# Performance work log

Hardware: AMD Instinct MI355X
Metric: run time of the kernel (lower is better)

Reference implementation:

```python
import jax, jax.numpy as jnp
import numpy as np

B, N, C, H = 1, 4096, 512, 8
S = 64  # sqrt(N), static


def setup_inputs() -> dict:
    key = jax.random.key(0)
    ks = jax.random.split(key, 4)
    d = C // H
    return {
        "x": jax.random.normal(ks[0], (B, N, C), dtype=jnp.float32),
        "num_heads": H,
        "bias": jnp.zeros((1,), dtype=jnp.float32),  # unused in original forward
        "scale": jnp.asarray(d ** -0.5, dtype=jnp.float32),
        "Wqkv": jax.random.normal(ks[1], (3 * C, C), dtype=jnp.float32) * (C ** -0.5),
        "bqkv": jnp.zeros((3 * C,), dtype=jnp.float32),
        "Wproj": jax.random.normal(ks[2], (C, C), dtype=jnp.float32) * (C ** -0.5),
        "bproj": jnp.zeros((C,), dtype=jnp.float32),
    }


def reference(x, num_heads, bias, scale, Wqkv, bqkv, Wproj, bproj):
    b, n, c = x.shape
    d = c // num_heads
    # fused QKV projection: [b, n, 3c] -> [3, b, h, n, d]
    qkv = (x @ Wqkv.T + bqkv).reshape(b, n, 3, num_heads, d).transpose(2, 0, 3, 1, 4)
    q, k, v = qkv[0] * scale, qkv[1], qkv[2]
    attn = jax.nn.softmax(jnp.einsum("bhnd,bhmd->bhnm", q, k), axis=-1)
    out = jnp.einsum("bhnm,bhmd->bhnd", attn, v)
    out = out.transpose(0, 2, 1, 3).reshape(b, n, c)
    out = out @ Wproj.T + bproj
    return out.reshape(b, S, S, c)
```

## Files before the change

kernel.cpp:

```cpp
#include <hip/hip_runtime.h>
#include <stdint.h>

#define NTOK 4096
#define CDIM 512
#define HEADS 8
#define DHEAD 64
#define PHEAD (NTOK * DHEAD)

typedef __bf16 bf16x8 __attribute__((ext_vector_type(8)));
typedef float f32x4 __attribute__((ext_vector_type(4)));

__device__ __forceinline__ unsigned short bfbits(float f) {
    return __builtin_bit_cast(unsigned short, (__bf16)f);
}

__device__ __forceinline__ f32x4 mfma32(bf16x8 a, bf16x8 b, f32x4 c) {
    return __builtin_amdgcn_mfma_f32_16x16x32_bf16(a, b, c, 0, 0, 0);
}

__global__ void cast3_k(const float* __restrict__ x, const float* __restrict__ wq,
                        const float* __restrict__ wp,
                        unsigned short* __restrict__ xb, unsigned short* __restrict__ wqb,
                        unsigned short* __restrict__ wpb) {
    const int b = blockIdx.x;
    const float* src; unsigned short* dst; int base;
    if (b < 2048)      { src = x;  dst = xb;  base = b * 1024; }
    else if (b < 2816) { src = wq; dst = wqb; base = (b - 2048) * 1024; }
    else               { src = wp; dst = wpb; base = (b - 2816) * 1024; }
    const int i = base + threadIdx.x * 4;
    const float4 v = *(const float4*)(src + i);
    ushort4 o;
    o.x = bfbits(v.x); o.y = bfbits(v.y); o.z = bfbits(v.z); o.w = bfbits(v.w);
    *(ushort4*)(dst + i) = o;
}

template<int MODE>
__global__ __launch_bounds__(256) void gemm_bt(
    const unsigned short* __restrict__ A,
    const unsigned short* __restrict__ Bm,
    const float* __restrict__ bias,
    const float* __restrict__ scale_p,
    unsigned short* __restrict__ qkv_out,
    float* __restrict__ c_out,
    int M, int Nn, int K)
{
    __shared__ __align__(16) unsigned short smem[64 * 136];
    unsigned short* lA = smem;
    unsigned short* lB = smem + 64 * 32;

    const int tid = threadIdx.x;
    const int mBase = blockIdx.y * 64, nBase = blockIdx.x * 128;
    const int lane = tid & 63, w = tid >> 6;
    const int l16 = lane & 15, quad = lane >> 4;

    f32x4 acc[4][2] = {};

    for (int kt = 0; kt < K; kt += 32) {
        __syncthreads();
        {
            const int fe = tid * 8;
            const int row = fe >> 5, col = fe & 31;
            *(uint4*)&lA[fe] = *(const uint4*)&A[(size_t)(mBase + row) * K + kt + col];
        }
#pragma unroll
        for (int i = 0; i < 2; ++i) {
            const int fe = (i * 256 + tid) * 8;
            const int row = fe >> 5, col = fe & 31;
            *(uint4*)&lB[fe] = *(const uint4*)&Bm[(size_t)(nBase + row) * K + kt + col];
        }
        __syncthreads();

        bf16x8 af[4], bfr[2];
#pragma unroll
        for (int i = 0; i < 4; ++i)
            af[i] = *(const bf16x8*)&lA[(i * 16 + l16) * 32 + quad * 8];
#pragma unroll
        for (int j = 0; j < 2; ++j)
            bfr[j] = *(const bf16x8*)&lB[(w * 32 + j * 16 + l16) * 32 + quad * 8];
#pragma unroll
        for (int i = 0; i < 4; ++i)
#pragma unroll
            for (int j = 0; j < 2; ++j)
                acc[i][j] = mfma32(af[i], bfr[j], acc[i][j]);
    }

    if (MODE == 1) {
#pragma unroll
        for (int i = 0; i < 4; ++i)
#pragma unroll
            for (int j = 0; j < 2; ++j)
#pragma unroll
                for (int r = 0; r < 4; ++r) {
                    const int grow = mBase + i * 16 + quad * 4 + r;
                    const int gcol = nBase + w * 32 + j * 16 + l16;
                    c_out[(size_t)grow * Nn + gcol] = acc[i][j][r] + bias[gcol];
                }
    } else {
        const int three = nBase >> 9;
        const float scl = scale_p[0] * 1.44269504f;
        const float mul = (three == 0) ? scl : 1.0f;

        __syncthreads();
#pragma unroll
        for (int i = 0; i < 4; ++i)
#pragma unroll
            for (int j = 0; j < 2; ++j)
#pragma unroll
                for (int r = 0; r < 4; ++r) {
                    const int rl = i * 16 + quad * 4 + r;
                    const int cl = w * 32 + j * 16 + l16;
                    const float v = (acc[i][j][r] + bias[nBase + cl]) * mul;
                    smem[rl * 136 + cl] = bfbits(v);
                }
        __syncthreads();

        const size_t base3 = (size_t)three * (PHEAD * HEADS);
        if (three < 2) {
#pragma unroll
            for (int pass = 0; pass < 4; ++pass) {
                const int idx = pass * 256 + tid;
                const int rl16 = idx & 15, qc = (idx >> 4) & 7;
                const int hsel = (idx >> 7) & 1, t16l = (idx >> 8) & 3;
                const uint4 d = *(const uint4*)&smem[(t16l * 16 + rl16) * 136 + hsel * 64 + qc * 8];
                const int hh = ((nBase >> 6) + hsel) & 7;
                const int t16 = (mBase >> 4) + t16l;
                const size_t dst = base3 + (size_t)hh * PHEAD +
                    (size_t)(((t16 * 2 + (qc >> 2)) * 64 + (qc & 3) * 16 + rl16) * 8);
                *(uint4*)&qkv_out[dst] = d;
            }
        } else {
#pragma unroll
            for (int pass = 0; pass < 4; ++pass) {
                const int idx = pass * 256 + tid;
                const int l16t = idx & 15, quadt = (idx >> 4) & 3;
                const int dt = (idx >> 6) & 3, k32l = (idx >> 8) & 1, hsel = (idx >> 9) & 1;
                const int col = hsel * 64 + dt * 16 + l16t;
                unsigned short o8[8];
#pragma unroll
                for (int e = 0; e < 4; ++e) {
                    o8[e]     = smem[(k32l * 32 + quadt * 4 + e) * 136 + col];
                    o8[e + 4] = smem[(k32l * 32 + 16 + quadt * 4 + e) * 136 + col];
                }
                const int hh = ((nBase >> 6) + hsel) & 7;
                const int k32 = (mBase >> 5) + k32l;
                const size_t dst = base3 + (size_t)hh * PHEAD +
                    (size_t)(((k32 * 4 + dt) * 64 + quadt * 16 + l16t) * 8);
                *(uint4*)&qkv_out[dst] = *(uint4*)o8;
            }
        }
    }
}

__global__ __launch_bounds__(256, 2) void flash4_k(
    const unsigned short* __restrict__ qf,
    const unsigned short* __restrict__ kf,
    const unsigned short* __restrict__ vf,
    unsigned short* __restrict__ attn_out)
{
    __shared__ float ldsO[4][32][68];
    __shared__ float sml[4][64];

    const int tid = threadIdx.x;
    const int lane = tid & 63;
    const int w = __builtin_amdgcn_readfirstlane(tid >> 6);
    const int l16 = lane & 15, quad = lane >> 4;
    const int h = blockIdx.x, qb = blockIdx.y;

    const unsigned short* qh = qf + (size_t)h * PHEAD;
    const unsigned short* kb = kf + (size_t)h * PHEAD + w * 4096;
    const unsigned short* vb = vf + (size_t)h * PHEAD + w * 4096;

    bf16x8 qfr[4][2];
#pragma unroll
    for (int qt = 0; qt < 4; ++qt)
#pragma unroll
        for (int ks = 0; ks < 2; ++ks)
            qfr[qt][ks] = *(const bf16x8*)&qh[((qb * 4 + qt) * 2 + ks) * 512 + lane * 8];

    bf16x8 ones;
#pragma unroll
    for (int j = 0; j < 8; ++j) ones[j] = (__bf16)1.0f;

    f32x4 oacc[4][4] = {};
    f32x4 lacc[4] = {};

#define KOFF(g) (((g) >> 1) * 16384 + ((g) & 1) * 2048)

    bf16x8 kA[4], kB[4];
#pragma unroll
    for (int i = 0; i < 4; ++i)
        kA[i] = *(const bf16x8*)&kb[KOFF(0) + i * 512 + lane * 8];

    auto body = [&](int g, bf16x8* kuse, bf16x8* kload) {
        const int gn = g + 1;
#pragma unroll
        for (int i = 0; i < 4; ++i)
            kload[i] = *(const bf16x8*)&kb[KOFF(gn) + i * 512 + lane * 8];
        bf16x8 vc[4];
#pragma unroll
        for (int i = 0; i < 4; ++i)
            vc[i] = *(const bf16x8*)&vb[KOFF(g) + i * 512 + lane * 8];

        f32x4 s[2][4];
#pragma unroll
        for (int kt = 0; kt < 2; ++kt)
#pragma unroll
            for (int qt = 0; qt < 4; ++qt) {
                f32x4 a = {};
                a = mfma32(kuse[kt * 2 + 0], qfr[qt][0], a);
                a = mfma32(kuse[kt * 2 + 1], qfr[qt][1], a);
                s[kt][qt] = a;
            }

        bf16x8 pf[4];
#pragma unroll
        for (int qt = 0; qt < 4; ++qt) {
            bf16x8 pb;
#pragma unroll
            for (int kt = 0; kt < 2; ++kt)
#pragma unroll
                for (int r = 0; r < 4; ++r)
                    pb[kt * 4 + r] = (__bf16)__builtin_amdgcn_exp2f(s[kt][qt][r]);
            pf[qt] = pb;
            lacc[qt] = mfma32(ones, pb, lacc[qt]);
        }
#pragma unroll
        for (int dt = 0; dt < 4; ++dt)
#pragma unroll
            for (int qt = 0; qt < 4; ++qt)
                oacc[dt][qt] = mfma32(vc[dt], pf[qt], oacc[dt][qt]);
    };

    for (int it = 0; it < 16; ++it) {
        body(it * 2 + 0, kA, kB);
        body(it * 2 + 1, kB, kA);
    }
#undef KOFF

    if (quad == 0) {
#pragma unroll
        for (int qt = 0; qt < 4; ++qt) sml[w][qt * 16 + l16] = lacc[qt][0];
    }

#pragma unroll
    for (int ph = 0; ph < 2; ++ph) {
        __syncthreads();
#pragma unroll
        for (int q2 = 0; q2 < 2; ++q2) {
            const int qt = ph * 2 + q2;
#pragma unroll
            for (int dt = 0; dt < 4; ++dt)
                *(f32x4*)&ldsO[w][q2 * 16 + l16][dt * 16 + quad * 4] = oacc[dt][qt];
        }
        __syncthreads();
        {
            const int q32 = tid >> 3, dseg = (tid & 7) * 8;
            const int q = ph * 32 + q32;
            const float L = sml[0][q] + sml[1][q] + sml[2][q] + sml[3][q];
            const float inv = 1.f / L;
            unsigned short o8[8];
#pragma unroll
            for (int i = 0; i < 8; ++i) {
                const float v = ldsO[0][q32][dseg + i] + ldsO[1][q32][dseg + i] +
                                ldsO[2][q32][dseg + i] + ldsO[3][q32][dseg + i];
                o8[i] = bfbits(v * inv);
            }
            *(uint4*)&attn_out[(size_t)(qb * 64 + q) * CDIM + h * DHEAD + dseg] = *(uint4*)o8;
        }
    }
}

extern "C" void kernel_launch(void* const* d_in, const int* in_sizes, int n_in,
                              void* d_out, int out_size, void* d_ws, size_t ws_size,
                              hipStream_t stream) {
    const float* x       = (const float*)d_in[0];
    const float* scale_p = (const float*)d_in[3];
    const float* Wqkv    = (const float*)d_in[4];
    const float* bqkv    = (const float*)d_in[5];
    const float* Wproj   = (const float*)d_in[6];
    const float* bproj   = (const float*)d_in[7];
    float* out = (float*)d_out;

    char* ws = (char*)d_ws;
    const size_t OFF_XB    = 0;
    const size_t OFF_WQKV  = OFF_XB + 4194304;
    const size_t OFF_WPROJ = OFF_WQKV + 1572864;
    const size_t OFF_QKV   = OFF_WPROJ + 524288;
    const size_t OFF_ATTN  = OFF_QKV + 12582912;
    const size_t NEEDED    = OFF_ATTN + 4194304;
    if (ws_size < NEEDED) return;

    unsigned short* xb     = (unsigned short*)(ws + OFF_XB);
    unsigned short* wqkvb  = (unsigned short*)(ws + OFF_WQKV);
    unsigned short* wprojb = (unsigned short*)(ws + OFF_WPROJ);
    unsigned short* qkvb   = (unsigned short*)(ws + OFF_QKV);
    unsigned short* attnb  = (unsigned short*)(ws + OFF_ATTN);

    cast3_k<<<3072, 256, 0, stream>>>(x, Wqkv, Wproj, xb, wqkvb, wprojb);

    gemm_bt<0><<<dim3(12, 64), 256, 0, stream>>>(xb, wqkvb, bqkv, scale_p,
                                                 qkvb, nullptr, NTOK, 3 * CDIM, CDIM);

    const unsigned short* qfr = qkvb;
    const unsigned short* kfr = qkvb + (size_t)PHEAD * HEADS;
    const unsigned short* vfr = qkvb + (size_t)2 * PHEAD * HEADS;
    flash4_k<<<dim3(8, 64), 256, 0, stream>>>(qfr, kfr, vfr, attnb);

    gemm_bt<1><<<dim3(4, 64), 256, 0, stream>>>(attnb, wprojb, bproj, nullptr,
                                                nullptr, out, NTOK, CDIM, CDIM);
}
```

Measured before the change: 159.3 us.

## Enlarge GEMM tiles with async LDS loads and split attention keys over eight waves

Measured after the change: 318.7 us. +100.1%, slower.

```diff
diff --git a/kernel.cpp b/kernel.cpp
--- a/kernel.cpp
+++ b/kernel.cpp
@@ -16,6 +16,12 @@
 
 __device__ __forceinline__ f32x4 mfma32(bf16x8 a, bf16x8 b, f32x4 c) {
     return __builtin_amdgcn_mfma_f32_16x16x32_bf16(a, b, c, 0, 0, 0);
+}
+
+__device__ __forceinline__ void async16(unsigned short* lds, const unsigned short* g) {
+    __builtin_amdgcn_global_load_lds(
+        (const __attribute__((address_space(1))) unsigned int*)g,
+        (__attribute__((address_space(3))) unsigned int*)lds, 16, 0, 0);
 }
 
 __global__ void cast3_k(const float* __restrict__ x, const float* __restrict__ wq,
@@ -35,7 +41,7 @@
 }
 
 template<int MODE>
-__global__ __launch_bounds__(256) void gemm_bt(
+__global__ __launch_bounds__(256) void gemm2(
     const unsigned short* __restrict__ A,
     const unsigned short* __restrict__ Bm,
     const float* __restrict__ bias,
@@ -44,43 +50,41 @@
     float* __restrict__ c_out,
     int M, int Nn, int K)
 {
-    __shared__ __align__(16) unsigned short smem[64 * 136];
+    __shared__ __align__(16) unsigned short smem[128 * 136];
     unsigned short* lA = smem;
-    unsigned short* lB = smem + 64 * 32;
+    unsigned short* lB = smem + 4096;
 
     const int tid = threadIdx.x;
-    const int mBase = blockIdx.y * 64, nBase = blockIdx.x * 128;
-    const int lane = tid & 63, w = tid >> 6;
+    const int mBase = blockIdx.y * 128, nBase = blockIdx.x * 128;
+    const int lane = tid & 63;
+    const int w = __builtin_amdgcn_readfirstlane(tid >> 6);
     const int l16 = lane & 15, quad = lane >> 4;
-
-    f32x4 acc[4][2] = {};
+    const int wr = (w >> 1) * 64, wc = (w & 1) * 64;
+    const int srow = lane >> 2, scol = (lane & 3) * 8;
+
+    f32x4 acc[4][4] = {};
 
     for (int kt = 0; kt < K; kt += 32) {
         __syncthreads();
-        {
-            const int fe = tid * 8;
-            const int row = fe >> 5, col = fe & 31;
-            *(uint4*)&lA[fe] = *(const uint4*)&A[(size_t)(mBase + row) * K + kt + col];
-        }
 #pragma unroll
         for (int i = 0; i < 2; ++i) {
-            const int fe = (i * 256 + tid) * 8;
-            const int row = fe >> 5, col = fe & 31;
-            *(uint4*)&lB[fe] = *(const uint4*)&Bm[(size_t)(nBase + row) * K + kt + col];
-        }
-        __syncthreads();
-
-        bf16x8 af[4], bfr[2];
-#pragma unroll
-        for (int i = 0; i < 4; ++i)
-            af[i] = *(const bf16x8*)&lA[(i * 16 + l16) * 32 + quad * 8];
-#pragma unroll
-        for (int j = 0; j < 2; ++j)
-            bfr[j] = *(const bf16x8*)&lB[(w * 32 + j * 16 + l16) * 32 + quad * 8];
-#pragma unroll
-        for (int i = 0; i < 4; ++i)
-#pragma unroll
-            for (int j = 0; j < 2; ++j)
+            const int r0 = (w * 2 + i) * 16;
+            async16(&lA[r0 * 32], &A[(size_t)(mBase + r0 + srow) * K + kt + scol]);
+            async16(&lB[r0 * 32], &Bm[(size_t)(nBase + r0 + srow) * K + kt + scol]);
+        }
+        __syncthreads();
+
+        bf16x8 af[4], bfr[4];
+#pragma unroll
+        for (int i = 0; i < 4; ++i)
+            af[i] = *(const bf16x8*)&lA[(wr + i * 16 + l16) * 32 + quad * 8];
+#pragma unroll
+        for (int j = 0; j < 4; ++j)
+            bfr[j] = *(const bf16x8*)&lB[(wc + j * 16 + l16) * 32 + quad * 8];
+#pragma unroll
+        for (int i = 0; i < 4; ++i)
+#pragma unroll
+            for (int j = 0; j < 4; ++j)
                 acc[i][j] = mfma32(af[i], bfr[j], acc[i][j]);
     }
 
@@ -88,11 +92,11 @@
 #pragma unroll
         for (int i = 0; i < 4; ++i)
 #pragma unroll
-            for (int j = 0; j < 2; ++j)
+            for (int j = 0; j < 4; ++j)
 #pragma unroll
                 for (int r = 0; r < 4; ++r) {
-                    const int grow = mBase + i * 16 + quad * 4 + r;
-                    const int gcol = nBase + w * 32 + j * 16 + l16;
+                    const int grow = mBase + wr + i * 16 + quad * 4 + r;
+                    const int gcol = nBase + wc + j * 16 + l16;
                     c_out[(size_t)grow * Nn + gcol] = acc[i][j][r] + bias[gcol];
                 }
     } else {
@@ -104,11 +108,11 @@
 #pragma unroll
         for (int i = 0; i < 4; ++i)
 #pragma unroll
-            for (int j = 0; j < 2; ++j)
+            for (int j = 0; j < 4; ++j)
 #pragma unroll
                 for (int r = 0; r < 4; ++r) {
-                    const int rl = i * 16 + quad * 4 + r;
-                    const int cl = w * 32 + j * 16 + l16;
+                    const int rl = wr + i * 16 + quad * 4 + r;
+                    const int cl = wc + j * 16 + l16;
                     const float v = (acc[i][j][r] + bias[nBase + cl]) * mul;
                     smem[rl * 136 + cl] = bfbits(v);
                 }
@@ -117,10 +121,10 @@
         const size_t base3 = (size_t)three * (PHEAD * HEADS);
         if (three < 2) {
 #pragma unroll
-            for (int pass = 0; pass < 4; ++pass) {
+            for (int pass = 0; pass < 8; ++pass) {
                 const int idx = pass * 256 + tid;
                 const int rl16 = idx & 15, qc = (idx >> 4) & 7;
-                const int hsel = (idx >> 7) & 1, t16l = (idx >> 8) & 3;
+                const int hsel = (idx >> 7) & 1, t16l = (idx >> 8) & 7;
                 const uint4 d = *(const uint4*)&smem[(t16l * 16 + rl16) * 136 + hsel * 64 + qc * 8];
                 const int hh = ((nBase >> 6) + hsel) & 7;
                 const int t16 = (mBase >> 4) + t16l;
@@ -130,10 +134,10 @@
             }
         } else {
 #pragma unroll
-            for (int pass = 0; pass < 4; ++pass) {
+            for (int pass = 0; pass < 8; ++pass) {
                 const int idx = pass * 256 + tid;
                 const int l16t = idx & 15, quadt = (idx >> 4) & 3;
-                const int dt = (idx >> 6) & 3, k32l = (idx >> 8) & 1, hsel = (idx >> 9) & 1;
+                const int dt = (idx >> 6) & 3, k32l = (idx >> 8) & 3, hsel = (idx >> 10) & 1;
                 const int col = hsel * 64 + dt * 16 + l16t;
                 unsigned short o8[8];
 #pragma unroll
@@ -151,14 +155,14 @@
     }
 }
 
-__global__ __launch_bounds__(256, 2) void flash4_k(
+__global__ __launch_bounds__(512, 4) void flash5_k(
     const unsigned short* __restrict__ qf,
     const unsigned short* __restrict__ kf,
     const unsigned short* __restrict__ vf,
     unsigned short* __restrict__ attn_out)
 {
-    __shared__ float ldsO[4][32][68];
-    __shared__ float sml[4][64];
+    __shared__ float ldsO[8][32][68];
+    __shared__ float sml[8][64];
 
     const int tid = threadIdx.x;
     const int lane = tid & 63;
@@ -167,8 +171,8 @@
     const int h = blockIdx.x, qb = blockIdx.y;
 
     const unsigned short* qh = qf + (size_t)h * PHEAD;
-    const unsigned short* kb = kf + (size_t)h * PHEAD + w * 4096;
-    const unsigned short* vb = vf + (size_t)h * PHEAD + w * 4096;
+    const unsigned short* kb = kf + (size_t)h * PHEAD + w * 32768;
+    const unsigned short* vb = vf + (size_t)h * PHEAD + w * 32768;
 
     bf16x8 qfr[4][2];
 #pragma unroll
@@ -184,22 +188,19 @@
     f32x4 oacc[4][4] = {};
     f32x4 lacc[4] = {};
 
-#define KOFF(g) (((g) >> 1) * 16384 + ((g) & 1) * 2048)
-
     bf16x8 kA[4], kB[4];
 #pragma unroll
     for (int i = 0; i < 4; ++i)
-        kA[i] = *(const bf16x8*)&kb[KOFF(0) + i * 512 + lane * 8];
+        kA[i] = *(const bf16x8*)&kb[i * 512 + lane * 8];
 
     auto body = [&](int g, bf16x8* kuse, bf16x8* kload) {
-        const int gn = g + 1;
-#pragma unroll
-        for (int i = 0; i < 4; ++i)
-            kload[i] = *(const bf16x8*)&kb[KOFF(gn) + i * 512 + lane * 8];
+#pragma unroll
+        for (int i = 0; i < 4; ++i)
+            kload[i] = *(const bf16x8*)&kb[(g + 1) * 2048 + i * 512 + lane * 8];
         bf16x8 vc[4];
 #pragma unroll
         for (int i = 0; i < 4; ++i)
-            vc[i] = *(const bf16x8*)&vb[KOFF(g) + i * 512 + lane * 8];
+            vc[i] = *(const bf16x8*)&vb[g * 2048 + i * 512 + lane * 8];
 
         f32x4 s[2][4];
 #pragma unroll
@@ -231,11 +232,10 @@
                 oacc[dt][qt] = mfma32(vc[dt], pf[qt], oacc[dt][qt]);
     };
 
-    for (int it = 0; it < 16; ++it) {
+    for (int it = 0; it < 8; ++it) {
         body(it * 2 + 0, kA, kB);
         body(it * 2 + 1, kB, kA);
     }
-#undef KOFF
 
     if (quad == 0) {
 #pragma unroll
@@ -253,16 +253,19 @@
                 *(f32x4*)&ldsO[w][q2 * 16 + l16][dt * 16 + quad * 4] = oacc[dt][qt];
         }
         __syncthreads();
-        {
+        if (tid < 256) {
             const int q32 = tid >> 3, dseg = (tid & 7) * 8;
             const int q = ph * 32 + q32;
-            const float L = sml[0][q] + sml[1][q] + sml[2][q] + sml[3][q];
+            float L = 0.f;
+#pragma unroll
+            for (int ww = 0; ww < 8; ++ww) L += sml[ww][q];
             const float inv = 1.f / L;
             unsigned short o8[8];
 #pragma unroll
             for (int i = 0; i < 8; ++i) {
-                const float v = ldsO[0][q32][dseg + i] + ldsO[1][q32][dseg + i] +
-                                ldsO[2][q32][dseg + i] + ldsO[3][q32][dseg + i];
+                float v = 0.f;
+#pragma unroll
+                for (int ww = 0; ww < 8; ++ww) v += ldsO[ww][q32][dseg + i];
                 o8[i] = bfbits(v * inv);
             }
             *(uint4*)&attn_out[(size_t)(qb * 64 + q) * CDIM + h * DHEAD + dseg] = *(uint4*)o8;
@@ -298,14 +301,14 @@
 
     cast3_k<<<3072, 256, 0, stream>>>(x, Wqkv, Wproj, xb, wqkvb, wprojb);
 
-    gemm_bt<0><<<dim3(12, 64), 256, 0, stream>>>(xb, wqkvb, bqkv, scale_p,
-                                                 qkvb, nullptr, NTOK, 3 * CDIM, CDIM);
+    gemm2<0><<<dim3(12, 32), 256, 0, stream>>>(xb, wqkvb, bqkv, scale_p,
+                                               qkvb, nullptr, NTOK, 3 * CDIM, CDIM);
 
     const unsigned short* qfr = qkvb;
     const unsigned short* kfr = qkvb + (size_t)PHEAD * HEADS;
     const unsigned short* vfr = qkvb + (size_t)2 * PHEAD * HEADS;
-    flash4_k<<<dim3(8, 64), 256, 0, stream>>>(qfr, kfr, vfr, attnb);
-
-    gemm_bt<1><<<dim3(4, 64), 256, 0, stream>>>(attnb, wprojb, bproj, nullptr,
-                                                nullptr, out, NTOK, CDIM, CDIM);
-}
+    flash5_k<<<dim3(8, 64), 512, 0, stream>>>(qfr, kfr, vfr, attnb);
+
+    gemm2<1><<<dim3(4, 32), 256, 0, stream>>>(attnb, wprojb, bproj, nullptr,
+                                              nullptr, out, NTOK, CDIM, CDIM);
+}
```
